# Kernel tuning notes

Measured on AMD Instinct MI355X. Metric: run time of the kernel, lower is better.

The kernel has to match this reference:

```python
import jax, jax.numpy as jnp
import numpy as np

B, S, D, H = 4, 2048, 512, 8
HD = D // H  # head_dim = 64


def setup_inputs() -> dict:
    key = jax.random.key(0)
    ks = jax.random.split(key, 10)
    scale = 1.0 / np.sqrt(D)  # keep activations O(1)
    x = jax.random.normal(ks[0], (B, S, D), dtype=jnp.float32)
    # causal mask, broadcast over batch and heads
    causal = jnp.tril(jnp.ones((S, S), dtype=bool))
    mask = jnp.broadcast_to(causal, (B, H, S, S))
    def lin(k):
        return jax.random.normal(k, (D, D), dtype=jnp.float32) * scale
    return {
        "x": x,
        "mask": mask,
        "Wq": lin(ks[1]), "bq": jax.random.normal(ks[2], (D,), dtype=jnp.float32) * 0.01,
        "Wk": lin(ks[3]), "bk": jax.random.normal(ks[4], (D,), dtype=jnp.float32) * 0.01,
        "Wv": lin(ks[5]), "bv": jax.random.normal(ks[6], (D,), dtype=jnp.float32) * 0.01,
        "Wo": lin(ks[7]), "bo": jax.random.normal(ks[8], (D,), dtype=jnp.float32) * 0.01,
    }


def reference(x, mask, Wq, bq, Wk, bk, Wv, bv, Wo, bo):
    # eqx.nn.Linear computes W @ x + b per row; batched form is x @ W.T + b.
    b, s, d = x.shape
    q = jnp.einsum("bsd,ed->bse", x, Wq) + bq
    k = jnp.einsum("bsd,ed->bse", x, Wk) + bk
    v = jnp.einsum("bsd,ed->bse", x, Wv) + bv
    # [B, H, S, HD]
    q = q.reshape(b, s, H, HD).transpose(0, 2, 1, 3)
    k = k.reshape(b, s, H, HD).transpose(0, 2, 1, 3)
    v = v.reshape(b, s, H, HD).transpose(0, 2, 1, 3)
    scores = jnp.einsum("bhqd,bhkd->bhqk", q, k) / jnp.sqrt(jnp.asarray(HD, x.dtype))
    scores = jnp.where(mask, scores, jnp.asarray(-1e9, x.dtype))
    attn = jax.nn.softmax(scores, axis=-1)
    attended = jnp.einsum("bhqk,bhkd->bhqd", attn, v)
    attended = attended.transpose(0, 2, 1, 3).reshape(b, s, d)
    out = jnp.einsum("bsd,ed->bse", attended, Wo) + bo
    return out
```

## Files before the change

### kernel.cpp

```cpp
#include <hip/hip_runtime.h>

#define S_LEN 2048
#define DM    512
#define NH    8
#define HD    64

typedef unsigned short u16;
typedef unsigned int   u32;
typedef __bf16 bf16_t;
typedef bf16_t bf16x8 __attribute__((ext_vector_type(8)));
typedef float  f32x4  __attribute__((ext_vector_type(4)));

__device__ __forceinline__ u16 f2bf(float f) {
    u32 u = __float_as_uint(f);
    u += 0x7FFFu + ((u >> 16) & 1u);
    return (u16)(u >> 16);
}

__device__ __forceinline__ void g2l16(const u16* g, u16* l) {
    __builtin_amdgcn_global_load_lds(
        (const __attribute__((address_space(1))) u32*)g,
        (__attribute__((address_space(3))) u32*)l,
        16, 0, 0);
}

__device__ __forceinline__ float qmax16(float v) {
    v = fmaxf(v, __shfl_xor(v, 1));
    v = fmaxf(v, __shfl_xor(v, 2));
    v = fmaxf(v, __shfl_xor(v, 4));
    v = fmaxf(v, __shfl_xor(v, 8));
    return v;
}
__device__ __forceinline__ float qsum16(float v) {
    v += __shfl_xor(v, 1);
    v += __shfl_xor(v, 2);
    v += __shfl_xor(v, 4);
    v += __shfl_xor(v, 8);
    return v;
}

__global__ __launch_bounds__(256) void cvt_bf16(
    const float* __restrict__ x,
    const float* __restrict__ wq, const float* __restrict__ wk,
    const float* __restrict__ wv, const float* __restrict__ wo,
    u16* __restrict__ xb, u16* __restrict__ wqb, u16* __restrict__ wkb,
    u16* __restrict__ wvb, u16* __restrict__ wob)
{
    const int y = blockIdx.y;
    const float* src; u16* dst; int n;
    if (y == 0)      { src = x;  dst = xb;  n = 4 * S_LEN * DM; }
    else if (y == 1) { src = wq; dst = wqb; n = DM * DM; }
    else if (y == 2) { src = wk; dst = wkb; n = DM * DM; }
    else if (y == 3) { src = wv; dst = wvb; n = DM * DM; }
    else             { src = wo; dst = wob; n = DM * DM; }
    int idx = (blockIdx.x * 256 + threadIdx.x) * 8;
    if (idx >= n) return;
    float4 f0 = *(const float4*)(src + idx);
    float4 f1 = *(const float4*)(src + idx + 4);
    u32 p0 = (u32)f2bf(f0.x) | ((u32)f2bf(f0.y) << 16);
    u32 p1 = (u32)f2bf(f0.z) | ((u32)f2bf(f0.w) << 16);
    u32 p2 = (u32)f2bf(f1.x) | ((u32)f2bf(f1.y) << 16);
    u32 p3 = (u32)f2bf(f1.z) | ((u32)f2bf(f1.w) << 16);
    *(uint4*)(dst + idx) = make_uint4(p0, p1, p2, p3);
}

__global__ __launch_bounds__(256) void qkv_gemm(
    const u16* __restrict__ xb,
    const u16* __restrict__ Wqb, const u16* __restrict__ Wkb, const u16* __restrict__ Wvb,
    const float* __restrict__ bq, const float* __restrict__ bk, const float* __restrict__ bv,
    u16* __restrict__ Qb, u16* __restrict__ Kb, u16* __restrict__ Vb)
{
    __shared__ u16 Als[2][4096];
    __shared__ u16 Bls[2][4096];

    const int t = threadIdx.x;
    const int lane = t & 63, w = t >> 6;
    const int ln = lane & 15, quad = lane >> 4;
    const int wm = w >> 1, wn = w & 1;
    const int m0 = blockIdx.x * 128;
    const int mat = blockIdx.y >> 2;
    const int n0 = (blockIdx.y & 3) * 128;

    const u16* __restrict__ Wb     = (mat == 0) ? Wqb : (mat == 1) ? Wkb : Wvb;
    const float* __restrict__ bias = (mat == 0) ? bq : (mat == 1) ? bk : bv;
    u16* __restrict__ outp         = (mat == 0) ? Qb : (mat == 1) ? Kb : Vb;
    const float qscale             = (mat == 0) ? 0.18033688f : 1.0f;

    const int ch0 = (w * 2 + 0) * 64 + lane;
    const int ch1 = (w * 2 + 1) * 64 + lane;
    const int sr0 = ch0 >> 2, sk0 = (ch0 & 3) ^ ((sr0 >> 1) & 3);
    const int sr1 = ch1 >> 2, sk1 = (ch1 & 3) ^ ((sr1 >> 1) & 3);
    const u16* pA0 = xb + (size_t)(m0 + sr0) * DM + sk0 * 8;
    const u16* pA1 = xb + (size_t)(m0 + sr1) * DM + sk1 * 8;
    const u16* pB0 = Wb + (size_t)(n0 + sr0) * DM + sk0 * 8;
    const u16* pB1 = Wb + (size_t)(n0 + sr1) * DM + sk1 * 8;
    const int lo0 = (w * 2 + 0) * 512;
    const int lo1 = (w * 2 + 1) * 512;

    g2l16(pA0, &Als[0][lo0]);
    g2l16(pA1, &Als[0][lo1]);
    g2l16(pB0, &Bls[0][lo0]);
    g2l16(pB1, &Bls[0][lo1]);

    f32x4 acc[4][4] = {};
    for (int it = 0; it < 16; ++it) {
        const int cur = it & 1, nxt = cur ^ 1;
        __syncthreads();
        if (it + 1 < 16) {
            const int k0n = (it + 1) * 32;
            g2l16(pA0 + k0n, &Als[nxt][lo0]);
            g2l16(pA1 + k0n, &Als[nxt][lo1]);
            g2l16(pB0 + k0n, &Bls[nxt][lo0]);
            g2l16(pB1 + k0n, &Bls[nxt][lo1]);
        }
        bf16x8 af[4], bf8[4];
        #pragma unroll
        for (int i = 0; i < 4; ++i) {
            int row = wm * 64 + i * 16 + ln;
            af[i] = *(const bf16x8*)(&Als[cur][0] + (row * 4 + (quad ^ ((row >> 1) & 3))) * 8);
        }
        #pragma unroll
        for (int j = 0; j < 4; ++j) {
            int row = wn * 64 + j * 16 + ln;
            bf8[j] = *(const bf16x8*)(&Bls[cur][0] + (row * 4 + (quad ^ ((row >> 1) & 3))) * 8);
        }
        #pragma unroll
        for (int i = 0; i < 4; ++i)
            #pragma unroll
            for (int j = 0; j < 4; ++j)
                acc[i][j] = __builtin_amdgcn_mfma_f32_16x16x32_bf16(af[i], bf8[j], acc[i][j], 0, 0, 0);
    }

    #pragma unroll
    for (int j = 0; j < 4; ++j) {
        int colg = n0 + wn * 64 + j * 16 + ln;
        float bj = bias[colg];
        int h = colg >> 6, d = colg & 63;
        #pragma unroll
        for (int i = 0; i < 4; ++i) {
            int mbase = m0 + wm * 64 + i * 16 + quad * 4;
            #pragma unroll
            for (int r = 0; r < 4; ++r) {
                int m = mbase + r;
                int bb = m >> 11, s = m & 2047;
                outp[(((size_t)bb * NH + h) * S_LEN + s) * HD + d] = f2bf((acc[i][j][r] + bj) * qscale);
            }
        }
    }
}

__global__ __launch_bounds__(256) void attn_mfma(
    const u16* __restrict__ Qb, const u16* __restrict__ Kb, const u16* __restrict__ Vb,
    u16* __restrict__ Attb)
{
    __shared__ u16 Qls[4096];
    __shared__ u16 Kls[2][4096];
    __shared__ u16 Vt[2][4096];
    __shared__ u16 Ps[4096];

    const int t = threadIdx.x;
    const int lane = t & 63, w = t >> 6;
    const int ln = lane & 15, quad = lane >> 4;
    const int bh = blockIdx.y;
    const int qt = (blockIdx.x + bh) & 31;
    const int q_base = qt * 64;
    const size_t base = (size_t)bh * S_LEN * HD;

    const int c0 = (w * 2 + 0) * 64 + lane;
    const int c1 = (w * 2 + 1) * 64 + lane;
    const int r0 = c0 >> 3, k0s = (c0 & 7) ^ (r0 & 7);
    const int r1 = c1 >> 3, k1s = (c1 & 7) ^ (r1 & 7);
    const int lo0 = (w * 2 + 0) * 512;
    const int lo1 = (w * 2 + 1) * 512;

    g2l16(Qb + base + (size_t)(q_base + r0) * HD + k0s * 8, Qls + lo0);
    g2l16(Qb + base + (size_t)(q_base + r1) * HD + k1s * 8, Qls + lo1);

    const u16* pK0 = Kb + base + (size_t)r0 * HD + k0s * 8;
    const u16* pK1 = Kb + base + (size_t)r1 * HD + k1s * 8;
    g2l16(pK0, &Kls[0][lo0]);
    g2l16(pK1, &Kls[0][lo1]);

    const int vkey0 = t >> 3, vd0 = (t & 7) * 8;
    const int vkey1 = (t + 256) >> 3;
    const u16* pV0 = Vb + base + (size_t)vkey0 * HD + vd0;
    const u16* pV1 = Vb + base + (size_t)vkey1 * HD + vd0;
    const int kvq0 = vkey0 >> 3, kvl0 = vkey0 & 7;
    const int kvq1 = vkey1 >> 3, kvl1 = vkey1 & 7;

    {
        uint4 vv0 = *(const uint4*)(pV0);
        uint4 vv1 = *(const uint4*)(pV1);
        u16 ve[8];
        *(uint4*)ve = vv0;
        #pragma unroll
        for (int ii = 0; ii < 8; ++ii) {
            int i = (ii + (t & 7)) & 7;
            int d = vd0 + i;
            Vt[0][(d * 8 + (kvq0 ^ (d & 7))) * 8 + kvl0] = ve[i];
        }
        *(uint4*)ve = vv1;
        #pragma unroll
        for (int ii = 0; ii < 8; ++ii) {
            int i = (ii + (t & 7)) & 7;
            int d = vd0 + i;
            Vt[0][(d * 8 + (kvq1 ^ (d & 7))) * 8 + kvl1] = ve[i];
        }
    }
    __syncthreads();

    bf16x8 aq[2];
    #pragma unroll
    for (int ks = 0; ks < 2; ++ks) {
        int row = w * 16 + ln;
        aq[ks] = *(const bf16x8*)(Qls + (row * 8 + ((ks * 4 + quad) ^ (row & 7))) * 8);
    }

    float m_st[4], l_st[4], alpha[4];
    f32x4 o[4] = {};
    #pragma unroll
    for (int r = 0; r < 4; ++r) { m_st[r] = -1e30f; l_st[r] = 0.f; }

    const int qrow_base = q_base + w * 16;

    for (int kt = 0; kt <= qt; ++kt) {
        const int cur = kt & 1, nxt = cur ^ 1;
        __syncthreads();

        uint4 vv0, vv1;
        const bool more = (kt < qt);
        if (more) {
            const size_t off = (size_t)(kt + 1) * 64 * HD;
            g2l16(pK0 + off, &Kls[nxt][lo0]);
            g2l16(pK1 + off, &Kls[nxt][lo1]);
            vv0 = *(const uint4*)(pV0 + off);
            vv1 = *(const uint4*)(pV1 + off);
        }

        f32x4 s[4] = {};
        #pragma unroll
        for (int ks = 0; ks < 2; ++ks)
            #pragma unroll
            for (int j = 0; j < 4; ++j) {
                int krow = j * 16 + ln;
                bf16x8 bk8 = *(const bf16x8*)(&Kls[cur][0] + (krow * 8 + ((ks * 4 + quad) ^ (krow & 7))) * 8);
                s[j] = __builtin_amdgcn_mfma_f32_16x16x32_bf16(aq[ks], bk8, s[j], 0, 0, 0);
            }

        if (more) {
            u16 ve[8];
            *(uint4*)ve = vv0;
            #pragma unroll
            for (int ii = 0; ii < 8; ++ii) {
                int i = (ii + (t & 7)) & 7;
                int d = vd0 + i;
                Vt[nxt][(d * 8 + (kvq0 ^ (d & 7))) * 8 + kvl0] = ve[i];
            }
            *(uint4*)ve = vv1;
            #pragma unroll
            for (int ii = 0; ii < 8; ++ii) {
                int i = (ii + (t & 7)) & 7;
                int d = vd0 + i;
                Vt[nxt][(d * 8 + (kvq1 ^ (d & 7))) * 8 + kvl1] = ve[i];
            }
        }

        if (kt == qt) {
            #pragma unroll
            for (int j = 0; j < 4; ++j)
                #pragma unroll
                for (int r = 0; r < 4; ++r) {
                    int qg = qrow_base + quad * 4 + r;
                    int kg = kt * 64 + j * 16 + ln;
                    if (kg > qg) s[j][r] = -1e30f;
                }
        }

        #pragma unroll
        for (int r = 0; r < 4; ++r) {
            float mx = fmaxf(fmaxf(s[0][r], s[1][r]), fmaxf(s[2][r], s[3][r]));
            mx = qmax16(mx);
            float mnew = fmaxf(m_st[r], mx);
            float al = __builtin_amdgcn_exp2f(m_st[r] - mnew);
            m_st[r] = mnew;
            float rs = 0.f;
            #pragma unroll
            for (int j = 0; j < 4; ++j) {
                float p = __builtin_amdgcn_exp2f(s[j][r] - mnew);
                s[j][r] = p;
                rs += p;
            }
            rs = qsum16(rs);
            l_st[r] = l_st[r] * al + rs;
            alpha[r] = al;
        }
        #pragma unroll
        for (int j = 0; j < 4; ++j)
            #pragma unroll
            for (int r = 0; r < 4; ++r)
                o[j][r] *= alpha[r];

        #pragma unroll
        for (int j = 0; j < 4; ++j) {
            int key = j * 16 + ln;
            int kq = key >> 3, kl = key & 7;
            #pragma unroll
            for (int r = 0; r < 4; ++r) {
                int qrow = w * 16 + quad * 4 + r;
                Ps[(qrow * 8 + (kq ^ (qrow & 7))) * 8 + kl] = f2bf(s[j][r]);
            }
        }

        #pragma unroll
        for (int ks = 0; ks < 2; ++ks) {
            int kqg = ks * 4 + quad;
            int prow = w * 16 + ln;
            bf16x8 pa = *(const bf16x8*)(Ps + (prow * 8 + (kqg ^ (prow & 7))) * 8);
            #pragma unroll
            for (int j = 0; j < 4; ++j) {
                int rowd = j * 16 + ln;
                bf16x8 vb8 = *(const bf16x8*)(&Vt[cur][0] + (rowd * 8 + (kqg ^ (rowd & 7))) * 8);
                o[j] = __builtin_amdgcn_mfma_f32_16x16x32_bf16(pa, vb8, o[j], 0, 0, 0);
            }
        }
    }

    const int bb = bh >> 3, h = bh & 7;
    #pragma unroll
    for (int r = 0; r < 4; ++r) {
        int qg = q_base + w * 16 + quad * 4 + r;
        float inv = 1.f / l_st[r];
        #pragma unroll
        for (int j = 0; j < 4; ++j) {
            int d = j * 16 + ln;
            Attb[((size_t)(bb * S_LEN + qg)) * DM + h * HD + d] = f2bf(o[j][r] * inv);
        }
    }
}

__global__ __launch_bounds__(256) void out_gemm(
    const u16* __restrict__ Ab, const u16* __restrict__ Wob,
    const float* __restrict__ bo, float* __restrict__ out)
{
    __shared__ u16 Als[2][2048];
    __shared__ u16 Bls[2][4096];

    const int t = threadIdx.x;
    const int lane = t & 63, w = t >> 6;
    const int ln = lane & 15, quad = lane >> 4;
    const int m0 = blockIdx.x * 64;
    const int n0 = blockIdx.y * 128;

    const int cha = w * 64 + lane;
    const int sra = cha >> 2, ska = (cha & 3) ^ ((sra >> 1) & 3);
    const u16* pA = Ab + (size_t)(m0 + sra) * DM + ska * 8;
    const int loa = w * 512;

    const int ch0 = (w * 2 + 0) * 64 + lane;
    const int ch1 = (w * 2 + 1) * 64 + lane;
    const int sr0 = ch0 >> 2, sk0 = (ch0 & 3) ^ ((sr0 >> 1) & 3);
    const int sr1 = ch1 >> 2, sk1 = (ch1 & 3) ^ ((sr1 >> 1) & 3);
    const u16* pB0 = Wob + (size_t)(n0 + sr0) * DM + sk0 * 8;
    const u16* pB1 = Wob + (size_t)(n0 + sr1) * DM + sk1 * 8;
    const int lo0 = (w * 2 + 0) * 512;
    const int lo1 = (w * 2 + 1) * 512;

    g2l16(pA,  &Als[0][loa]);
    g2l16(pB0, &Bls[0][lo0]);
    g2l16(pB1, &Bls[0][lo1]);

    f32x4 acc[4][2] = {};
    for (int it = 0; it < 16; ++it) {
        const int cur = it & 1, nxt = cur ^ 1;
        __syncthreads();
        if (it + 1 < 16) {
            const int k0n = (it + 1) * 32;
            g2l16(pA + k0n,  &Als[nxt][loa]);
            g2l16(pB0 + k0n, &Bls[nxt][lo0]);
            g2l16(pB1 + k0n, &Bls[nxt][lo1]);
        }
        bf16x8 af[4], bf8[2];
        #pragma unroll
        for (int i = 0; i < 4; ++i) {
            int row = i * 16 + ln;
            af[i] = *(const bf16x8*)(&Als[cur][0] + (row * 4 + (quad ^ ((row >> 1) & 3))) * 8);
        }
        #pragma unroll
        for (int j = 0; j < 2; ++j) {
            int row = w * 32 + j * 16 + ln;
            bf8[j] = *(const bf16x8*)(&Bls[cur][0] + (row * 4 + (quad ^ ((row >> 1) & 3))) * 8);
        }
        #pragma unroll
        for (int i = 0; i < 4; ++i)
            #pragma unroll
            for (int j = 0; j < 2; ++j)
                acc[i][j] = __builtin_amdgcn_mfma_f32_16x16x32_bf16(af[i], bf8[j], acc[i][j], 0, 0, 0);
    }

    #pragma unroll
    for (int j = 0; j < 2; ++j) {
        int colg = n0 + w * 32 + j * 16 + ln;
        float bj = bo[colg];
        #pragma unroll
        for (int i = 0; i < 4; ++i) {
            int mbase = m0 + i * 16 + quad * 4;
            #pragma unroll
            for (int r = 0; r < 4; ++r) {
                int m = mbase + r;
                out[(size_t)m * DM + colg] = acc[i][j][r] + bj;
            }
        }
    }
}

extern "C" void kernel_launch(void* const* d_in, const int* in_sizes, int n_in,
                              void* d_out, int out_size, void* d_ws, size_t ws_size,
                              hipStream_t stream) {
    const float* x  = (const float*)d_in[0];
    const float* Wq = (const float*)d_in[2];
    const float* bq = (const float*)d_in[3];
    const float* Wk = (const float*)d_in[4];
    const float* bk = (const float*)d_in[5];
    const float* Wv = (const float*)d_in[6];
    const float* bv = (const float*)d_in[7];
    const float* Wo = (const float*)d_in[8];
    const float* bo = (const float*)d_in[9];
    float* out = (float*)d_out;

    u16* ws = (u16*)d_ws;
    const size_t NX = (size_t)4 * S_LEN * DM;
    const size_t NW = (size_t)DM * DM;
    u16* xb   = ws;
    u16* wqb  = xb + NX;
    u16* wkb  = wqb + NW;
    u16* wvb  = wkb + NW;
    u16* wob  = wvb + NW;
    u16* Qb   = wob + NW;
    u16* Kb   = Qb + NX;
    u16* Vb   = Kb + NX;
    u16* Attb = Vb + NX;

    cvt_bf16<<<dim3(2048, 5), 256, 0, stream>>>(x, Wq, Wk, Wv, Wo, xb, wqb, wkb, wvb, wob);
    qkv_gemm<<<dim3(64, 12), 256, 0, stream>>>(xb, wqb, wkb, wvb, bq, bk, bv, Qb, Kb, Vb);
    attn_mfma<<<dim3(32, 32), 256, 0, stream>>>(Qb, Kb, Vb, Attb);
    out_gemm<<<dim3(128, 4), 256, 0, stream>>>(Attb, wob, bo, out);
}
```

Measured before the change: 754.9 us.

## Write V transposed in projection kernel and load it asynchronously into LDS

```diff
diff --git a/kernel.cpp b/kernel.cpp
--- a/kernel.cpp
+++ b/kernel.cpp
@@ -143,7 +143,12 @@
             for (int r = 0; r < 4; ++r) {
                 int m = mbase + r;
                 int bb = m >> 11, s = m & 2047;
-                outp[(((size_t)bb * NH + h) * S_LEN + s) * HD + d] = f2bf((acc[i][j][r] + bj) * qscale);
+                float v = (acc[i][j][r] + bj) * qscale;
+                if (mat == 2) {
+                    outp[(((size_t)bb * NH + h) * HD + d) * S_LEN + s] = f2bf(v);
+                } else {
+                    outp[(((size_t)bb * NH + h) * S_LEN + s) * HD + d] = f2bf(v);
+                }
             }
         }
     }
@@ -181,32 +186,11 @@
     g2l16(pK0, &Kls[0][lo0]);
     g2l16(pK1, &Kls[0][lo1]);
 
-    const int vkey0 = t >> 3, vd0 = (t & 7) * 8;
-    const int vkey1 = (t + 256) >> 3;
-    const u16* pV0 = Vb + base + (size_t)vkey0 * HD + vd0;
-    const u16* pV1 = Vb + base + (size_t)vkey1 * HD + vd0;
-    const int kvq0 = vkey0 >> 3, kvl0 = vkey0 & 7;
-    const int kvq1 = vkey1 >> 3, kvl1 = vkey1 & 7;
-
-    {
-        uint4 vv0 = *(const uint4*)(pV0);
-        uint4 vv1 = *(const uint4*)(pV1);
-        u16 ve[8];
-        *(uint4*)ve = vv0;
-        #pragma unroll
-        for (int ii = 0; ii < 8; ++ii) {
-            int i = (ii + (t & 7)) & 7;
-            int d = vd0 + i;
-            Vt[0][(d * 8 + (kvq0 ^ (d & 7))) * 8 + kvl0] = ve[i];
-        }
-        *(uint4*)ve = vv1;
-        #pragma unroll
-        for (int ii = 0; ii < 8; ++ii) {
-            int i = (ii + (t & 7)) & 7;
-            int d = vd0 + i;
-            Vt[0][(d * 8 + (kvq1 ^ (d & 7))) * 8 + kvl1] = ve[i];
-        }
-    }
+    const u16* pV0 = Vb + base + (size_t)r0 * S_LEN + k0s * 8;
+    const u16* pV1 = Vb + base + (size_t)r1 * S_LEN + k1s * 8;
+    g2l16(pV0, &Vt[0][lo0]);
+    g2l16(pV1, &Vt[0][lo1]);
+
     __syncthreads();
 
     bf16x8 aq[2];
@@ -227,14 +211,13 @@
         const int cur = kt & 1, nxt = cur ^ 1;
         __syncthreads();
 
-        uint4 vv0, vv1;
-        const bool more = (kt < qt);
-        if (more) {
-            const size_t off = (size_t)(kt + 1) * 64 * HD;
-            g2l16(pK0 + off, &Kls[nxt][lo0]);
-            g2l16(pK1 + off, &Kls[nxt][lo1]);
-            vv0 = *(const uint4*)(pV0 + off);
-            vv1 = *(const uint4*)(pV1 + off);
+        if (kt < qt) {
+            const size_t offK = (size_t)(kt + 1) * 64 * HD;
+            const size_t offV = (size_t)(kt + 1) * 64;
+            g2l16(pK0 + offK, &Kls[nxt][lo0]);
+            g2l16(pK1 + offK, &Kls[nxt][lo1]);
+            g2l16(pV0 + offV, &Vt[nxt][lo0]);
+            g2l16(pV1 + offV, &Vt[nxt][lo1]);
         }
 
         f32x4 s[4] = {};
@@ -246,24 +229,6 @@
                 bf16x8 bk8 = *(const bf16x8*)(&Kls[cur][0] + (krow * 8 + ((ks * 4 + quad) ^ (krow & 7))) * 8);
                 s[j] = __builtin_amdgcn_mfma_f32_16x16x32_bf16(aq[ks], bk8, s[j], 0, 0, 0);
             }
-
-        if (more) {
-            u16 ve[8];
-            *(uint4*)ve = vv0;
-            #pragma unroll
-            for (int ii = 0; ii < 8; ++ii) {
-                int i = (ii + (t & 7)) & 7;
-                int d = vd0 + i;
-                Vt[nxt][(d * 8 + (kvq0 ^ (d & 7))) * 8 + kvl0] = ve[i];
-            }
-            *(uint4*)ve = vv1;
-            #pragma unroll
-            for (int ii = 0; ii < 8; ++ii) {
-                int i = (ii + (t & 7)) & 7;
-                int d = vd0 + i;
-                Vt[nxt][(d * 8 + (kvq1 ^ (d & 7))) * 8 + kvl1] = ve[i];
-            }
-        }
 
         if (kt == qt) {
             #pragma unroll
@@ -313,13 +278,12 @@
 
         #pragma unroll
         for (int ks = 0; ks < 2; ++ks) {
-            int kqg = ks * 4 + quad;
             int prow = w * 16 + ln;
-            bf16x8 pa = *(const bf16x8*)(Ps + (prow * 8 + (kqg ^ (prow & 7))) * 8);
+            bf16x8 pa = *(const bf16x8*)(Ps + (prow * 8 + ((ks * 4 + quad) ^ (prow & 7))) * 8);
             #pragma unroll
             for (int j = 0; j < 4; ++j) {
                 int rowd = j * 16 + ln;
-                bf16x8 vb8 = *(const bf16x8*)(&Vt[cur][0] + (rowd * 8 + (kqg ^ (rowd & 7))) * 8);
+                bf16x8 vb8 = *(const bf16x8*)(&Vt[cur][0] + (rowd * 8 + ((ks * 4 + quad) ^ (rowd & 7))) * 8);
                 o[j] = __builtin_amdgcn_mfma_f32_16x16x32_bf16(pa, vb8, o[j], 0, 0, 0);
             }
         }
```

Result: faster. 735.1 us (-2.6%).
